# Optimization experiments

Hardware: AMD Instinct MI355X
Metric: run time of the kernel (lower is better)

## Reference

```python
import jax, jax.numpy as jnp
import numpy as np

PAIR = 128
HID = 64
EPS = 1e-5


def _ln(x, w, b):
    mu = jnp.mean(x, axis=-1, keepdims=True)
    var = jnp.mean((x - mu) ** 2, axis=-1, keepdims=True)
    return (x - mu) * jax.lax.rsqrt(var + EPS) * w + b


def setup_inputs() -> dict:
    key = jax.random.key(0)
    ks = jax.random.split(key, 8)
    B, N = 1, 448
    s_in = 1.0 / np.sqrt(PAIR)
    s_h = 1.0 / np.sqrt(HID)
    return {
        "z": jax.random.normal(ks[0], (B, N, N, PAIR), jnp.float32),
        "z_mask": jnp.ones((B, N, N), jnp.float32),
        "ln_w": jnp.ones((PAIR,), jnp.float32),
        "ln_b": jnp.zeros((PAIR,), jnp.float32),
        "lnh_w": jnp.ones((HID,), jnp.float32),
        "lnh_b": jnp.zeros((HID,), jnp.float32),
        "g1_w": jax.random.uniform(ks[1], (PAIR, HID), jnp.float32, -s_in, s_in),
        "g1_b": jnp.zeros((HID,), jnp.float32),
        "g2_w": jax.random.uniform(ks[2], (PAIR, HID), jnp.float32, -s_in, s_in),
        "g2_b": jnp.zeros((HID,), jnp.float32),
        "l1_w": jax.random.uniform(ks[3], (PAIR, HID), jnp.float32, -s_in, s_in),
        "l1_b": jnp.zeros((HID,), jnp.float32),
        "l2_w": jax.random.uniform(ks[4], (PAIR, HID), jnp.float32, -s_in, s_in),
        "l2_b": jnp.zeros((HID,), jnp.float32),
        "eg_w": jax.random.uniform(ks[5], (PAIR, PAIR), jnp.float32, -s_in, s_in),
        "eg_b": jnp.zeros((PAIR,), jnp.float32),
        "out_w": jax.random.uniform(ks[6], (HID, PAIR), jnp.float32, -s_h, s_h),
        "out_b": jnp.zeros((PAIR,), jnp.float32),
    }


def reference(z, z_mask, ln_w, ln_b, lnh_w, lnh_b, g1_w, g1_b, g2_w, g2_b,
              l1_w, l1_b, l2_w, l2_b, eg_w, eg_b, out_w, out_b):
    m = z_mask[..., None]                      # [B,N,N,1]
    zn = _ln(z, ln_w, ln_b)                    # [B,N,N,P]
    ab1 = jax.nn.sigmoid(zn @ g1_w + g1_b) * (zn @ l1_w + l1_b) * m  # [B,N,N,H]
    ab2 = jax.nn.sigmoid(zn @ g2_w + g2_b) * (zn @ l2_w + l2_b) * m  # [B,N,N,H]
    # outgoing + incoming triangle products, per channel c
    block = (jnp.einsum('bikc,bjkc->bijc', ab1, ab2)
             + jnp.einsum('bkic,bkjc->bijc', ab1, ab2))              # [B,N,N,H]
    out = jax.nn.sigmoid(zn @ eg_w + eg_b) * (_ln(block, lnh_w, lnh_b) @ out_w + out_b) * m
    return out
```

## Files before the change

### kernel.cpp

```cpp
#include <hip/hip_runtime.h>
#include <stdint.h>

#define N 448
#define NN (N*N)
#define P 128
#define H 64
#define PN 512
#define CH (PN*N)

typedef __attribute__((ext_vector_type(8))) short bf16x8;
typedef __attribute__((ext_vector_type(4))) float f32x4;
typedef __attribute__((ext_vector_type(16))) float f32x16;

__device__ __forceinline__ ushort f2bf(float f) {
    uint u = __builtin_bit_cast(uint, f);
    uint r = u + 0x7FFFu + ((u >> 16) & 1u);
    return (ushort)(r >> 16);
}
__device__ __forceinline__ float bf2f(ushort h) {
    uint u = ((uint)h) << 16;
    return __builtin_bit_cast(float, u);
}
__device__ __forceinline__ float sigmoidf(float x) {
    return 1.0f / (1.0f + __expf(-x));
}
__device__ __forceinline__ uint cvtpk(float lo, float hi) {
    uint r;
    asm("v_cvt_pk_bf16_f32 %0, %1, %2" : "=v"(r) : "v"(lo), "v"(hi));
    return r;
}

__global__ void k_prep(const float* __restrict__ g1w, const float* __restrict__ l1w,
                       const float* __restrict__ g2w, const float* __restrict__ l2w,
                       const float* __restrict__ egw,
                       ushort* __restrict__ wfrag) {
    int idx = blockIdx.x*256 + threadIdx.x;
    for (int e = idx; e < 24*4*64*8; e += gridDim.x*256) {
        int b  = e & 7;
        int l  = (e >> 3) & 63;
        int ks = (e >> 9) & 3;
        int ct = e >> 11;
        int k   = ks*32 + 8*(l>>4) + b;
        int col = ct*16 + (l & 15);
        float v;
        if (col < 64)       v = g1w[k*64 + col];
        else if (col < 128) v = l1w[k*64 + col - 64];
        else if (col < 192) v = g2w[k*64 + col - 128];
        else if (col < 256) v = l2w[k*64 + col - 192];
        else                v = egw[k*128 + col - 256];
        wfrag[e] = f2bf(v);
    }
}

__global__ __launch_bounds__(256) void k_proj(
    const float* __restrict__ z, const float* __restrict__ mask,
    const float* __restrict__ lnw, const float* __restrict__ lnb,
    const float* __restrict__ g1b, const float* __restrict__ l1b,
    const float* __restrict__ g2b, const float* __restrict__ l2b,
    const float* __restrict__ egb,
    const ushort* __restrict__ wfrag,
    ushort* __restrict__ abt, ushort* __restrict__ gsig)
{
    __shared__ ushort zn[64*128];
    __shared__ ushort abstage[128*72];
    const int t = threadIdx.x;
    const int w = t >> 6, l = t & 63;
    const int i = blockIdx.x / 7, j0 = (blockIdx.x % 7) * 64;

    {
        const int p = t >> 2;
        const int q = t & 3;
        const float* zp = z + (size_t)(i*N + j0 + p)*P + q*32;
        float4 v[8];
        #pragma unroll
        for (int x = 0; x < 8; ++x) v[x] = *(const float4*)(zp + x*4);
        float s = 0.f, sq = 0.f;
        #pragma unroll
        for (int x = 0; x < 8; ++x) {
            s  += v[x].x + v[x].y + v[x].z + v[x].w;
            sq += v[x].x*v[x].x + v[x].y*v[x].y + v[x].z*v[x].z + v[x].w*v[x].w;
        }
        s += __shfl_xor(s, 1);  sq += __shfl_xor(sq, 1);
        s += __shfl_xor(s, 2);  sq += __shfl_xor(sq, 2);
        float mu   = s * (1.0f/128.0f);
        float var  = sq * (1.0f/128.0f) - mu*mu;
        float rstd = rsqrtf(var + 1e-5f);
        #pragma unroll
        for (int cc = 0; cc < 4; ++cc) {
            int chunk = q*4 + cc;
            const float* lwp = lnw + chunk*8;
            const float* lbp = lnb + chunk*8;
            float4 lwa = *(const float4*)(lwp), lwb = *(const float4*)(lwp+4);
            float4 lba = *(const float4*)(lbp), lbb = *(const float4*)(lbp+4);
            float4 va = v[cc*2], vb = v[cc*2+1];
            float n0 = (va.x - mu)*rstd*lwa.x + lba.x;
            float n1 = (va.y - mu)*rstd*lwa.y + lba.y;
            float n2 = (va.z - mu)*rstd*lwa.z + lba.z;
            float n3 = (va.w - mu)*rstd*lwa.w + lba.w;
            float n4 = (vb.x - mu)*rstd*lwb.x + lbb.x;
            float n5 = (vb.y - mu)*rstd*lwb.y + lbb.y;
            float n6 = (vb.z - mu)*rstd*lwb.z + lbb.z;
            float n7 = (vb.w - mu)*rstd*lwb.w + lbb.w;
            uint4 pk;
            pk.x = cvtpk(n0, n1);
            pk.y = cvtpk(n2, n3);
            pk.z = cvtpk(n4, n5);
            pk.w = cvtpk(n6, n7);
            uint boff = (uint)p*256u + (((uint)(chunk ^ (p & 7)) & 15u) << 4);
            *(uint4*)((char*)zn + boff) = pk;
        }
    }
    __syncthreads();

    const int half = w & 1, pair = w >> 1;
    const uint lr = l & 15, lk = l >> 4;
    const float* mrow = mask + (size_t)i*N + j0;
    const float* gb = pair ? g2b : g1b;
    const float* lb = pair ? l2b : l1b;

    float4 mv4[4];
    #pragma unroll
    for (int mi = 0; mi < 4; ++mi) mv4[mi] = *(const float4*)(mrow + mi*16 + (int)lk*4);

    #pragma unroll 1
    for (int sub = 0; sub < 2; ++sub) {
        const int ctg = pair*8 + half*2 + sub;
        const int ctl = ctg + 4;
        f32x4 ag[4], al[4];
        #pragma unroll
        for (int mi = 0; mi < 4; ++mi) { ag[mi] = (f32x4){0,0,0,0}; al[mi] = (f32x4){0,0,0,0}; }

        #pragma unroll
        for (int ks = 0; ks < 4; ++ks) {
            bf16x8 bg  = *(const bf16x8*)(wfrag + ((size_t)(ctg*4 + ks)*64 + l)*8);
            bf16x8 blf = *(const bf16x8*)(wfrag + ((size_t)(ctl*4 + ks)*64 + l)*8);
            #pragma unroll
            for (int mi = 0; mi < 4; ++mi) {
                uint row = mi*16u + lr;
                uint chunk = (uint)(ks*4) + lk;
                bf16x8 af = *(const bf16x8*)((const char*)zn + row*256u + (((chunk ^ (row & 7u)) & 15u) << 4));
                ag[mi] = __builtin_amdgcn_mfma_f32_16x16x32_bf16(af, bg,  ag[mi], 0,0,0);
                al[mi] = __builtin_amdgcn_mfma_f32_16x16x32_bf16(af, blf, al[mi], 0,0,0);
            }
        }

        const int cidx = (half*2 + sub)*16 + (int)lr;
        const float gbias = gb[cidx];
        const float lbias = lb[cidx];
        const int srow = pair*64 + cidx;
        #pragma unroll
        for (int mi = 0; mi < 4; ++mi) {
            float4 mv = mv4[mi];
            float o0 = sigmoidf(ag[mi][0] + gbias) * (al[mi][0] + lbias) * mv.x;
            float o1 = sigmoidf(ag[mi][1] + gbias) * (al[mi][1] + lbias) * mv.y;
            float o2 = sigmoidf(ag[mi][2] + gbias) * (al[mi][2] + lbias) * mv.z;
            float o3 = sigmoidf(ag[mi][3] + gbias) * (al[mi][3] + lbias) * mv.w;
            uint2 pk;
            pk.x = cvtpk(o0, o1);
            pk.y = cvtpk(o2, o3);
            *(uint2*)(abstage + (size_t)srow*72 + mi*16 + (int)lk*4) = pk;
        }
    }
    __syncthreads();

    {
        int r = t >> 1, hh2 = t & 1;
        const ushort* sp = abstage + (size_t)r*72 + hh2*32;
        ushort* dp = abt + (size_t)r*CH + (size_t)i*N + j0 + hh2*32;
        #pragma unroll
        for (int k2 = 0; k2 < 4; ++k2) {
            uint4 vv = *(const uint4*)(sp + k2*8);
            *(uint4*)(dp + k2*8) = vv;
        }
    }

    {
        f32x4 ae[4][2];
        #pragma unroll
        for (int mi = 0; mi < 4; ++mi) { ae[mi][0] = (f32x4){0,0,0,0}; ae[mi][1] = (f32x4){0,0,0,0}; }

        #pragma unroll
        for (int ks = 0; ks < 4; ++ks) {
            bf16x8 b0 = *(const bf16x8*)(wfrag + ((size_t)((16 + w*2)*4 + ks)*64 + l)*8);
            bf16x8 b1 = *(const bf16x8*)(wfrag + ((size_t)((17 + w*2)*4 + ks)*64 + l)*8);
            #pragma unroll
            for (int mi = 0; mi < 4; ++mi) {
                uint row = mi*16u + lr;
                uint chunk = (uint)(ks*4) + lk;
                bf16x8 af = *(const bf16x8*)((const char*)zn + row*256u + (((chunk ^ (row & 7u)) & 15u) << 4));
                ae[mi][0] = __builtin_amdgcn_mfma_f32_16x16x32_bf16(af, b0, ae[mi][0], 0,0,0);
                ae[mi][1] = __builtin_amdgcn_mfma_f32_16x16x32_bf16(af, b1, ae[mi][1], 0,0,0);
            }
        }

        __syncthreads();

        float biasB[2];
        biasB[0] = egb[w*32 + (int)lr];
        biasB[1] = egb[w*32 + 16 + (int)lr];
        #pragma unroll
        for (int mi = 0; mi < 4; ++mi) {
            float4 mv = mv4[mi];
            float mva[4] = { mv.x, mv.y, mv.z, mv.w };
            #pragma unroll
            for (int e = 0; e < 2; ++e) {
                uint cg = (uint)(w*32 + e*16) + lr;
                #pragma unroll
                for (int r = 0; r < 4; ++r) {
                    float sg = sigmoidf(ae[mi][e][r] + biasB[e]) * mva[r];
                    uint row = (uint)(mi*16) + lk*4u + (uint)r;
                    uint boff = row*256u + (((((cg >> 3) ^ (row & 7u)) & 15u)) << 4) + ((cg & 7u) << 1);
                    *(ushort*)((char*)zn + boff) = (ushort)cvtpk(sg, sg);
                }
            }
        }
    }
    __syncthreads();

    {
        int p2 = t >> 2, q2 = t & 3;
        size_t pos = (size_t)(i*N + j0 + p2);
        #pragma unroll
        for (int s2 = 0; s2 < 4; ++s2) {
            int chunk = q2*4 + s2;
            uint boff = (uint)p2*256u + (((uint)(chunk ^ (p2 & 7)) & 15u) << 4);
            uint4 vv = *(const uint4*)((const char*)zn + boff);
            *(uint4*)(gsig + pos*128 + q2*32 + s2*8) = vv;
        }
    }
}

__global__ __launch_bounds__(256) void k_transpose(const ushort* __restrict__ abt,
                                                   ushort* __restrict__ abtt) {
    int bid = blockIdx.x;
    int tile = bid % 49, a = bid / 49;
    int y0 = (tile / 7) * 64, x0 = (tile % 7) * 64;
    const ushort* src = abt  + (size_t)a*CH;
    ushort*       dst = abtt + (size_t)a*CH;
    __shared__ ushort tl[64][68];
    int t = threadIdx.x;
    #pragma unroll
    for (int q = 0; q < 4; ++q) {
        int f = q*1024 + t*4;
        int r = f >> 6, c4 = f & 63;
        ushort4 v = *(const ushort4*)(src + (size_t)(y0 + r)*N + x0 + c4);
        tl[r][c4] = v.x; tl[r][c4+1] = v.y; tl[r][c4+2] = v.z; tl[r][c4+3] = v.w;
    }
    __syncthreads();
    #pragma unroll
    for (int q = 0; q < 4; ++q) {
        int f = q*1024 + t*4;
        int r = f >> 6, c4 = f & 63;
        ushort4 v;
        v.x = tl[c4][r]; v.y = tl[c4+1][r]; v.z = tl[c4+2][r]; v.w = tl[c4+3][r];
        *(ushort4*)(dst + (size_t)(x0 + r)*N + y0 + c4) = v;
    }
}

__global__ __launch_bounds__(256) void k_tri(const ushort* __restrict__ abt,
                                             const ushort* __restrict__ abtt,
                                             float* __restrict__ blk) {
    int bid = (blockIdx.x & 7)*128 + (blockIdx.x >> 3);
    const int c = bid >> 4;
    const int tij = bid & 15;
    const int i0 = (tij >> 2) * 128, j0 = (tij & 3) * 128;
    const int t = threadIdx.x, w = t >> 6, l = t & 63;
    const int wr = w >> 1, wc = w & 1;
    const uint l31 = l & 31, kg = (uint)l >> 5;

    __shared__ ushort lds[4][128*64];

    const ushort* basep = (w >= 2) ? abtt : abt;
    const int chan = (w & 1) ? 64 + c : c;
    const int r0   = (w & 1) ? j0 : i0;
    const ushort* sbase = basep + (size_t)chan*CH + (size_t)r0*N;

    f32x16 acc[2][2];
    #pragma unroll
    for (int a = 0; a < 2; ++a)
        #pragma unroll
        for (int b = 0; b < 2; ++b) acc[a][b] = (f32x16){0,0,0,0,0,0,0,0,0,0,0,0,0,0,0,0};

    for (int kk = 0; kk < 7; ++kk) {
        __syncthreads();
        const ushort* sb = sbase + kk*64;
        #pragma unroll
        for (int q = 0; q < 16; ++q) {
            int r  = q*8 + (l >> 3);
            int ch = (l & 7) ^ (r & 7);
            const ushort* g = sb + (size_t)r*N + ch*8;
            __builtin_amdgcn_global_load_lds(
                (const __attribute__((address_space(1))) uint*)g,
                (__attribute__((address_space(3))) uint*)(&lds[w][q*512]),
                16, 0, 0);
        }
        __syncthreads();

        #pragma unroll
        for (int ks = 0; ks < 4; ++ks) {
            const uint chunk = (uint)(ks*2) + kg;
            {
                bf16x8 aA[2], bB[2];
                #pragma unroll
                for (int x = 0; x < 2; ++x) {
                    uint rowa = (uint)wr*64u + (uint)x*32u + l31;
                    uint rowb = (uint)wc*64u + (uint)x*32u + l31;
                    aA[x] = *(const bf16x8*)((const char*)lds[0] + rowa*128u + (((chunk ^ (rowa & 7u)) & 15u) << 4));
                    bB[x] = *(const bf16x8*)((const char*)lds[1] + rowb*128u + (((chunk ^ (rowb & 7u)) & 15u) << 4));
                }
                #pragma unroll
                for (int ra = 0; ra < 2; ++ra)
                    #pragma unroll
                    for (int cb = 0; cb < 2; ++cb)
                        acc[ra][cb] = __builtin_amdgcn_mfma_f32_32x32x16_bf16(aA[ra], bB[cb], acc[ra][cb], 0,0,0);
            }
            {
                bf16x8 aA[2], bB[2];
                #pragma unroll
                for (int x = 0; x < 2; ++x) {
                    uint rowa = (uint)wr*64u + (uint)x*32u + l31;
                    uint rowb = (uint)wc*64u + (uint)x*32u + l31;
                    aA[x] = *(const bf16x8*)((const char*)lds[2] + rowa*128u + (((chunk ^ (rowa & 7u)) & 15u) << 4));
                    bB[x] = *(const bf16x8*)((const char*)lds[3] + rowb*128u + (((chunk ^ (rowb & 7u)) & 15u) << 4));
                }
                #pragma unroll
                for (int ra = 0; ra < 2; ++ra)
                    #pragma unroll
                    for (int cb = 0; cb < 2; ++cb)
                        acc[ra][cb] = __builtin_amdgcn_mfma_f32_32x32x16_bf16(aA[ra], bB[cb], acc[ra][cb], 0,0,0);
            }
        }
    }

    #pragma unroll
    for (int ra = 0; ra < 2; ++ra) {
        #pragma unroll
        for (int cb = 0; cb < 2; ++cb) {
            int jb = j0 + wc*64 + cb*32 + (int)l31;
            if (jb < N) {
                #pragma unroll
                for (int r = 0; r < 16; ++r) {
                    int ii = i0 + wr*64 + ra*32 + (r & 3) + 8*(r >> 2) + 4*(int)kg;
                    if (ii < N) blk[(size_t)c*NN + (size_t)ii*N + jb] = acc[ra][cb][r];
                }
            }
        }
    }
}

__global__ __launch_bounds__(256) void k_out(const float* __restrict__ blk,
    const ushort* __restrict__ gsig,
    const float* __restrict__ lnhw, const float* __restrict__ lnhb,
    const float* __restrict__ outw, const float* __restrict__ outb,
    float* __restrict__ out)
{
    __shared__ float sblk[2][64][68];
    const int t = threadIdx.x;
    const int w = t >> 6, l = t & 63;
    const int base = blockIdx.x * 256;

    float4 pre[4];
    #pragma unroll
    for (int qq = 0; qq < 4; ++qq) {
        int flat = qq*256 + t;
        int h = flat >> 4, f4 = flat & 15;
        pre[qq] = *(const float4*)(blk + (size_t)h*NN + base + f4*4);
    }

    #pragma unroll 1
    for (int tt = 0; tt < 4; ++tt) {
        const int b = tt & 1;
        const int pos0 = base + tt*64;

        #pragma unroll
        for (int qq = 0; qq < 4; ++qq) {
            int flat = qq*256 + t;
            int h = flat >> 4, f4 = flat & 15;
            sblk[b][f4*4+0][h] = pre[qq].x;
            sblk[b][f4*4+1][h] = pre[qq].y;
            sblk[b][f4*4+2][h] = pre[qq].z;
            sblk[b][f4*4+3][h] = pre[qq].w;
        }
        if (tt < 3) {
            #pragma unroll
            for (int qq = 0; qq < 4; ++qq) {
                int flat = qq*256 + t;
                int h = flat >> 4, f4 = flat & 15;
                pre[qq] = *(const float4*)(blk + (size_t)h*NN + pos0 + 64 + f4*4);
            }
        }
        __syncthreads();

        {
            int p = w*16 + (l >> 2);
            int sub = l & 3;
            float vv[16];
            float s = 0.f, sq = 0.f;
            #pragma unroll
            for (int j = 0; j < 16; ++j) {
                float x = sblk[b][p][sub*16 + j];
                vv[j] = x; s += x; sq += x*x;
            }
            s += __shfl_xor(s, 1);  sq += __shfl_xor(sq, 1);
            s += __shfl_xor(s, 2);  sq += __shfl_xor(sq, 2);
            float mu   = s * (1.0f/64.0f);
            float var  = sq * (1.0f/64.0f) - mu*mu;
            float rstd = rsqrtf(var + 1e-5f);
            #pragma unroll
            for (int j = 0; j < 16; ++j) {
                float nv = (vv[j] - mu)*rstd*lnhw[sub*16+j] + lnhb[sub*16+j];
                sblk[b][p][sub*16 + j] = nv;
            }
        }
        __syncthreads();

        const int c4 = (t & 31) * 4;
        const int pg = t >> 5;
        float4 ob = *(const float4*)(outb + c4);

        #pragma unroll 1
        for (int hh = 0; hh < 2; ++hh) {
            const int prow = hh*32 + pg*4;
            float acc[4][4];
            #pragma unroll
            for (int j2 = 0; j2 < 4; ++j2)
                #pragma unroll
                for (int cc = 0; cc < 4; ++cc) acc[j2][cc] = 0.f;

            #pragma unroll 4
            for (int h4 = 0; h4 < 16; ++h4) {
                float4 wv[4];
                #pragma unroll
                for (int j = 0; j < 4; ++j)
                    wv[j] = *(const float4*)(outw + (h4*4+j)*128 + c4);
                #pragma unroll
                for (int j2 = 0; j2 < 4; ++j2) {
                    float4 av = *(const float4*)(&sblk[b][prow + j2][h4*4]);
                    acc[j2][0] += av.x*wv[0].x + av.y*wv[1].x + av.z*wv[2].x + av.w*wv[3].x;
                    acc[j2][1] += av.x*wv[0].y + av.y*wv[1].y + av.z*wv[2].y + av.w*wv[3].y;
                    acc[j2][2] += av.x*wv[0].z + av.y*wv[1].z + av.z*wv[2].z + av.w*wv[3].z;
                    acc[j2][3] += av.x*wv[0].w + av.y*wv[1].w + av.z*wv[2].w + av.w*wv[3].w;
                }
            }

            #pragma unroll
            for (int j2 = 0; j2 < 4; ++j2) {
                size_t pos = (size_t)(pos0 + prow + j2);
                ushort4 gv = *(const ushort4*)(gsig + pos*128 + c4);
                float4 res;
                res.x = bf2f(gv.x) * (acc[j2][0] + ob.x);
                res.y = bf2f(gv.y) * (acc[j2][1] + ob.y);
                res.z = bf2f(gv.z) * (acc[j2][2] + ob.z);
                res.w = bf2f(gv.w) * (acc[j2][3] + ob.w);
                *(float4*)(out + pos*128 + c4) = res;
            }
        }
    }
}

extern "C" void kernel_launch(void* const* d_in, const int* in_sizes, int n_in,
                              void* d_out, int out_size, void* d_ws, size_t ws_size,
                              hipStream_t stream) {
    const float* z    = (const float*)d_in[0];
    const float* mask = (const float*)d_in[1];
    const float* lnw  = (const float*)d_in[2];
    const float* lnb  = (const float*)d_in[3];
    const float* lnhw = (const float*)d_in[4];
    const float* lnhb = (const float*)d_in[5];
    const float* g1w  = (const float*)d_in[6];
    const float* g1b  = (const float*)d_in[7];
    const float* g2w  = (const float*)d_in[8];
    const float* g2b  = (const float*)d_in[9];
    const float* l1w  = (const float*)d_in[10];
    const float* l1b  = (const float*)d_in[11];
    const float* l2w  = (const float*)d_in[12];
    const float* l2b  = (const float*)d_in[13];
    const float* egw  = (const float*)d_in[14];
    const float* egb  = (const float*)d_in[15];
    const float* outw = (const float*)d_in[16];
    const float* outb = (const float*)d_in[17];

    char* ws = (char*)d_ws;
    const size_t SZ_AB = (size_t)2*64*CH*2;
    const size_t SZ_G  = (size_t)NN*128*2;
    const size_t SZ_BL = (size_t)64*NN*4;
    ushort* abt    = (ushort*)ws;
    ushort* abtt   = (ushort*)(ws + SZ_AB);
    ushort* gsig   = (ushort*)(ws + 2*SZ_AB);
    float*  blkb   = (float*) (ws + 2*SZ_AB + SZ_G);
    ushort* wfrag  = (ushort*)(ws + 2*SZ_AB + SZ_G + SZ_BL);

    k_prep<<<32, 256, 0, stream>>>(g1w, l1w, g2w, l2w, egw, wfrag);
    k_proj<<<3136, 256, 0, stream>>>(z, mask, lnw, lnb, g1b, l1b, g2b, l2b, egb, wfrag, abt, gsig);
    k_transpose<<<128*49, 256, 0, stream>>>(abt, abtt);
    k_tri<<<64*16, 256, 0, stream>>>(abt, abtt, blkb);
    k_out<<<NN/256, 256, 0, stream>>>(blkb, gsig, lnhw, lnhb, outw, outb, (float*)d_out);
}
```

Measured before the change: 290.2 us.

## Make k_proj persistent per row with register prefetch of next z tile

k_proj now launches one block per row i (448 blocks) and loops over the 7 column tiles internally, instead of one block per 64-column tile. The next tile's z values are loaded into registers while the current tile is normalized and projected, and the LayerNorm weights and eg bias are loaded once per block. The aim is to hide global load latency and amortize per-block setup. The cost is fewer blocks (448 on a many-CU GPU, so lower occupancy and parallelism), an extra barrier per iteration, and higher register pressure from the prefetch buffer.

```diff
diff --git a/kernel.cpp b/kernel.cpp
--- a/kernel.cpp
+++ b/kernel.cpp
@@ -65,168 +65,187 @@
     __shared__ ushort abstage[128*72];
     const int t = threadIdx.x;
     const int w = t >> 6, l = t & 63;
-    const int i = blockIdx.x / 7, j0 = (blockIdx.x % 7) * 64;
-
-    {
-        const int p = t >> 2;
-        const int q = t & 3;
-        const float* zp = z + (size_t)(i*N + j0 + p)*P + q*32;
-        float4 v[8];
-        #pragma unroll
-        for (int x = 0; x < 8; ++x) v[x] = *(const float4*)(zp + x*4);
-        float s = 0.f, sq = 0.f;
-        #pragma unroll
-        for (int x = 0; x < 8; ++x) {
-            s  += v[x].x + v[x].y + v[x].z + v[x].w;
-            sq += v[x].x*v[x].x + v[x].y*v[x].y + v[x].z*v[x].z + v[x].w*v[x].w;
-        }
-        s += __shfl_xor(s, 1);  sq += __shfl_xor(sq, 1);
-        s += __shfl_xor(s, 2);  sq += __shfl_xor(sq, 2);
-        float mu   = s * (1.0f/128.0f);
-        float var  = sq * (1.0f/128.0f) - mu*mu;
-        float rstd = rsqrtf(var + 1e-5f);
-        #pragma unroll
-        for (int cc = 0; cc < 4; ++cc) {
-            int chunk = q*4 + cc;
-            const float* lwp = lnw + chunk*8;
-            const float* lbp = lnb + chunk*8;
-            float4 lwa = *(const float4*)(lwp), lwb = *(const float4*)(lwp+4);
-            float4 lba = *(const float4*)(lbp), lbb = *(const float4*)(lbp+4);
-            float4 va = v[cc*2], vb = v[cc*2+1];
-            float n0 = (va.x - mu)*rstd*lwa.x + lba.x;
-            float n1 = (va.y - mu)*rstd*lwa.y + lba.y;
-            float n2 = (va.z - mu)*rstd*lwa.z + lba.z;
-            float n3 = (va.w - mu)*rstd*lwa.w + lba.w;
-            float n4 = (vb.x - mu)*rstd*lwb.x + lbb.x;
-            float n5 = (vb.y - mu)*rstd*lwb.y + lbb.y;
-            float n6 = (vb.z - mu)*rstd*lwb.z + lbb.z;
-            float n7 = (vb.w - mu)*rstd*lwb.w + lbb.w;
-            uint4 pk;
-            pk.x = cvtpk(n0, n1);
-            pk.y = cvtpk(n2, n3);
-            pk.z = cvtpk(n4, n5);
-            pk.w = cvtpk(n6, n7);
-            uint boff = (uint)p*256u + (((uint)(chunk ^ (p & 7)) & 15u) << 4);
-            *(uint4*)((char*)zn + boff) = pk;
-        }
-    }
-    __syncthreads();
-
+    const int i = blockIdx.x;
+
+    const int p = t >> 2;
+    const int q = t & 3;
     const int half = w & 1, pair = w >> 1;
     const uint lr = l & 15, lk = l >> 4;
-    const float* mrow = mask + (size_t)i*N + j0;
     const float* gb = pair ? g2b : g1b;
     const float* lb = pair ? l2b : l1b;
 
-    float4 mv4[4];
+    float4 lwa[4], lwb[4], lba[4], lbb[4];
     #pragma unroll
-    for (int mi = 0; mi < 4; ++mi) mv4[mi] = *(const float4*)(mrow + mi*16 + (int)lk*4);
+    for (int cc = 0; cc < 4; ++cc) {
+        int chunk = q*4 + cc;
+        lwa[cc] = *(const float4*)(lnw + chunk*8);
+        lwb[cc] = *(const float4*)(lnw + chunk*8 + 4);
+        lba[cc] = *(const float4*)(lnb + chunk*8);
+        lbb[cc] = *(const float4*)(lnb + chunk*8 + 4);
+    }
+    float egb0 = egb[w*32 + (int)lr];
+    float egb1 = egb[w*32 + 16 + (int)lr];
+
+    float4 vA[8];
+    {
+        const float* zp = z + (size_t)(i*N + p)*P + q*32;
+        #pragma unroll
+        for (int x = 0; x < 8; ++x) vA[x] = *(const float4*)(zp + x*4);
+    }
 
     #pragma unroll 1
-    for (int sub = 0; sub < 2; ++sub) {
-        const int ctg = pair*8 + half*2 + sub;
-        const int ctl = ctg + 4;
-        f32x4 ag[4], al[4];
-        #pragma unroll
-        for (int mi = 0; mi < 4; ++mi) { ag[mi] = (f32x4){0,0,0,0}; al[mi] = (f32x4){0,0,0,0}; }
-
-        #pragma unroll
-        for (int ks = 0; ks < 4; ++ks) {
-            bf16x8 bg  = *(const bf16x8*)(wfrag + ((size_t)(ctg*4 + ks)*64 + l)*8);
-            bf16x8 blf = *(const bf16x8*)(wfrag + ((size_t)(ctl*4 + ks)*64 + l)*8);
+    for (int jt = 0; jt < 7; ++jt) {
+        const int j0 = jt*64;
+        const float* mrow = mask + (size_t)i*N + j0;
+
+        {
+            float s = 0.f, sq = 0.f;
+            #pragma unroll
+            for (int x = 0; x < 8; ++x) {
+                s  += vA[x].x + vA[x].y + vA[x].z + vA[x].w;
+                sq += vA[x].x*vA[x].x + vA[x].y*vA[x].y + vA[x].z*vA[x].z + vA[x].w*vA[x].w;
+            }
+            s += __shfl_xor(s, 1);  sq += __shfl_xor(sq, 1);
+            s += __shfl_xor(s, 2);  sq += __shfl_xor(sq, 2);
+            float mu   = s * (1.0f/128.0f);
+            float var  = sq * (1.0f/128.0f) - mu*mu;
+            float rstd = rsqrtf(var + 1e-5f);
+            #pragma unroll
+            for (int cc = 0; cc < 4; ++cc) {
+                int chunk = q*4 + cc;
+                float4 va = vA[cc*2], vb = vA[cc*2+1];
+                float n0 = (va.x - mu)*rstd*lwa[cc].x + lba[cc].x;
+                float n1 = (va.y - mu)*rstd*lwa[cc].y + lba[cc].y;
+                float n2 = (va.z - mu)*rstd*lwa[cc].z + lba[cc].z;
+                float n3 = (va.w - mu)*rstd*lwa[cc].w + lba[cc].w;
+                float n4 = (vb.x - mu)*rstd*lwb[cc].x + lbb[cc].x;
+                float n5 = (vb.y - mu)*rstd*lwb[cc].y + lbb[cc].y;
+                float n6 = (vb.z - mu)*rstd*lwb[cc].z + lbb[cc].z;
+                float n7 = (vb.w - mu)*rstd*lwb[cc].w + lbb[cc].w;
+                uint4 pk;
+                pk.x = cvtpk(n0, n1);
+                pk.y = cvtpk(n2, n3);
+                pk.z = cvtpk(n4, n5);
+                pk.w = cvtpk(n6, n7);
+                uint boff = (uint)p*256u + (((uint)(chunk ^ (p & 7)) & 15u) << 4);
+                *(uint4*)((char*)zn + boff) = pk;
+            }
+        }
+        if (jt < 6) {
+            const float* zp = z + (size_t)(i*N + j0 + 64 + p)*P + q*32;
+            #pragma unroll
+            for (int x = 0; x < 8; ++x) vA[x] = *(const float4*)(zp + x*4);
+        }
+        __syncthreads();
+
+        float4 mv4[4];
+        #pragma unroll
+        for (int mi = 0; mi < 4; ++mi) mv4[mi] = *(const float4*)(mrow + mi*16 + (int)lk*4);
+
+        #pragma unroll 1
+        for (int sub = 0; sub < 2; ++sub) {
+            const int ctg = pair*8 + half*2 + sub;
+            const int ctl = ctg + 4;
+            f32x4 ag[4], al[4];
+            #pragma unroll
+            for (int mi = 0; mi < 4; ++mi) { ag[mi] = (f32x4){0,0,0,0}; al[mi] = (f32x4){0,0,0,0}; }
+
+            #pragma unroll
+            for (int ks = 0; ks < 4; ++ks) {
+                bf16x8 bg  = *(const bf16x8*)(wfrag + ((size_t)(ctg*4 + ks)*64 + l)*8);
+                bf16x8 blf = *(const bf16x8*)(wfrag + ((size_t)(ctl*4 + ks)*64 + l)*8);
+                #pragma unroll
+                for (int mi = 0; mi < 4; ++mi) {
+                    uint row = mi*16u + lr;
+                    uint chunk = (uint)(ks*4) + lk;
+                    bf16x8 af = *(const bf16x8*)((const char*)zn + row*256u + (((chunk ^ (row & 7u)) & 15u) << 4));
+                    ag[mi] = __builtin_amdgcn_mfma_f32_16x16x32_bf16(af, bg,  ag[mi], 0,0,0);
+                    al[mi] = __builtin_amdgcn_mfma_f32_16x16x32_bf16(af, blf, al[mi], 0,0,0);
+                }
+            }
+
+            const int cidx = (half*2 + sub)*16 + (int)lr;
+            const float gbias = gb[cidx];
+            const float lbias = lb[cidx];
+            const int srow = pair*64 + cidx;
             #pragma unroll
             for (int mi = 0; mi < 4; ++mi) {
-                uint row = mi*16u + lr;
-                uint chunk = (uint)(ks*4) + lk;
-                bf16x8 af = *(const bf16x8*)((const char*)zn + row*256u + (((chunk ^ (row & 7u)) & 15u) << 4));
-                ag[mi] = __builtin_amdgcn_mfma_f32_16x16x32_bf16(af, bg,  ag[mi], 0,0,0);
-                al[mi] = __builtin_amdgcn_mfma_f32_16x16x32_bf16(af, blf, al[mi], 0,0,0);
-            }
-        }
-
-        const int cidx = (half*2 + sub)*16 + (int)lr;
-        const float gbias = gb[cidx];
-        const float lbias = lb[cidx];
-        const int srow = pair*64 + cidx;
-        #pragma unroll
-        for (int mi = 0; mi < 4; ++mi) {
-            float4 mv = mv4[mi];
-            float o0 = sigmoidf(ag[mi][0] + gbias) * (al[mi][0] + lbias) * mv.x;
-            float o1 = sigmoidf(ag[mi][1] + gbias) * (al[mi][1] + lbias) * mv.y;
-            float o2 = sigmoidf(ag[mi][2] + gbias) * (al[mi][2] + lbias) * mv.z;
-            float o3 = sigmoidf(ag[mi][3] + gbias) * (al[mi][3] + lbias) * mv.w;
-            uint2 pk;
-            pk.x = cvtpk(o0, o1);
-            pk.y = cvtpk(o2, o3);
-            *(uint2*)(abstage + (size_t)srow*72 + mi*16 + (int)lk*4) = pk;
-        }
-    }
-    __syncthreads();
-
-    {
-        int r = t >> 1, hh2 = t & 1;
-        const ushort* sp = abstage + (size_t)r*72 + hh2*32;
-        ushort* dp = abt + (size_t)r*CH + (size_t)i*N + j0 + hh2*32;
-        #pragma unroll
-        for (int k2 = 0; k2 < 4; ++k2) {
-            uint4 vv = *(const uint4*)(sp + k2*8);
-            *(uint4*)(dp + k2*8) = vv;
-        }
-    }
-
-    {
-        f32x4 ae[4][2];
-        #pragma unroll
-        for (int mi = 0; mi < 4; ++mi) { ae[mi][0] = (f32x4){0,0,0,0}; ae[mi][1] = (f32x4){0,0,0,0}; }
-
-        #pragma unroll
-        for (int ks = 0; ks < 4; ++ks) {
-            bf16x8 b0 = *(const bf16x8*)(wfrag + ((size_t)((16 + w*2)*4 + ks)*64 + l)*8);
-            bf16x8 b1 = *(const bf16x8*)(wfrag + ((size_t)((17 + w*2)*4 + ks)*64 + l)*8);
+                float4 mv = mv4[mi];
+                float o0 = sigmoidf(ag[mi][0] + gbias) * (al[mi][0] + lbias) * mv.x;
+                float o1 = sigmoidf(ag[mi][1] + gbias) * (al[mi][1] + lbias) * mv.y;
+                float o2 = sigmoidf(ag[mi][2] + gbias) * (al[mi][2] + lbias) * mv.z;
+                float o3 = sigmoidf(ag[mi][3] + gbias) * (al[mi][3] + lbias) * mv.w;
+                uint2 pk;
+                pk.x = cvtpk(o0, o1);
+                pk.y = cvtpk(o2, o3);
+                *(uint2*)(abstage + (size_t)srow*72 + mi*16 + (int)lk*4) = pk;
+            }
+        }
+        __syncthreads();
+
+        {
+            int r = t >> 1, hh2 = t & 1;
+            const ushort* sp = abstage + (size_t)r*72 + hh2*32;
+            ushort* dp = abt + (size_t)r*CH + (size_t)i*N + j0 + hh2*32;
+            #pragma unroll
+            for (int k2 = 0; k2 < 4; ++k2) {
+                uint4 vv = *(const uint4*)(sp + k2*8);
+                *(uint4*)(dp + k2*8) = vv;
+            }
+        }
+
+        {
+            f32x4 ae[4][2];
+            #pragma unroll
+            for (int mi = 0; mi < 4; ++mi) { ae[mi][0] = (f32x4){0,0,0,0}; ae[mi][1] = (f32x4){0,0,0,0}; }
+
+            #pragma unroll
+            for (int ks = 0; ks < 4; ++ks) {
+                bf16x8 b0 = *(const bf16x8*)(wfrag + ((size_t)((16 + w*2)*4 + ks)*64 + l)*8);
+                bf16x8 b1 = *(const bf16x8*)(wfrag + ((size_t)((17 + w*2)*4 + ks)*64 + l)*8);
+                #pragma unroll
+                for (int mi = 0; mi < 4; ++mi) {
+                    uint row = mi*16u + lr;
+                    uint chunk = (uint)(ks*4) + lk;
+                    bf16x8 af = *(const bf16x8*)((const char*)zn + row*256u + (((chunk ^ (row & 7u)) & 15u) << 4));
+                    ae[mi][0] = __builtin_amdgcn_mfma_f32_16x16x32_bf16(af, b0, ae[mi][0], 0,0,0);
+                    ae[mi][1] = __builtin_amdgcn_mfma_f32_16x16x32_bf16(af, b1, ae[mi][1], 0,0,0);
+                }
+            }
+
+            __syncthreads();
+
             #pragma unroll
             for (int mi = 0; mi < 4; ++mi) {
-                uint row = mi*16u + lr;
-                uint chunk = (uint)(ks*4) + lk;
-                bf16x8 af = *(const bf16x8*)((const char*)zn + row*256u + (((chunk ^ (row & 7u)) & 15u) << 4));
-                ae[mi][0] = __builtin_amdgcn_mfma_f32_16x16x32_bf16(af, b0, ae[mi][0], 0,0,0);
-                ae[mi][1] = __builtin_amdgcn_mfma_f32_16x16x32_bf16(af, b1, ae[mi][1], 0,0,0);
-            }
-        }
-
-        __syncthreads();
-
-        float biasB[2];
-        biasB[0] = egb[w*32 + (int)lr];
-        biasB[1] = egb[w*32 + 16 + (int)lr];
-        #pragma unroll
-        for (int mi = 0; mi < 4; ++mi) {
-            float4 mv = mv4[mi];
-            float mva[4] = { mv.x, mv.y, mv.z, mv.w };
-            #pragma unroll
-            for (int e = 0; e < 2; ++e) {
-                uint cg = (uint)(w*32 + e*16) + lr;
-                #pragma unroll
-                for (int r = 0; r < 4; ++r) {
-                    float sg = sigmoidf(ae[mi][e][r] + biasB[e]) * mva[r];
-                    uint row = (uint)(mi*16) + lk*4u + (uint)r;
-                    uint boff = row*256u + (((((cg >> 3) ^ (row & 7u)) & 15u)) << 4) + ((cg & 7u) << 1);
-                    *(ushort*)((char*)zn + boff) = (ushort)cvtpk(sg, sg);
-                }
-            }
-        }
-    }
-    __syncthreads();
-
-    {
-        int p2 = t >> 2, q2 = t & 3;
-        size_t pos = (size_t)(i*N + j0 + p2);
-        #pragma unroll
-        for (int s2 = 0; s2 < 4; ++s2) {
-            int chunk = q2*4 + s2;
-            uint boff = (uint)p2*256u + (((uint)(chunk ^ (p2 & 7)) & 15u) << 4);
-            uint4 vv = *(const uint4*)((const char*)zn + boff);
-            *(uint4*)(gsig + pos*128 + q2*32 + s2*8) = vv;
-        }
+                float4 mv = mv4[mi];
+                float mva[4] = { mv.x, mv.y, mv.z, mv.w };
+                #pragma unroll
+                for (int e = 0; e < 2; ++e) {
+                    uint cg = (uint)(w*32 + e*16) + lr;
+                    float bias = e ? egb1 : egb0;
+                    #pragma unroll
+                    for (int r = 0; r < 4; ++r) {
+                        float sg = sigmoidf(ae[mi][e][r] + bias) * mva[r];
+                        uint row = (uint)(mi*16) + lk*4u + (uint)r;
+                        uint boff = row*256u + (((((cg >> 3) ^ (row & 7u)) & 15u)) << 4) + ((cg & 7u) << 1);
+                        *(ushort*)((char*)zn + boff) = (ushort)cvtpk(sg, sg);
+                    }
+                }
+            }
+        }
+        __syncthreads();
+
+        {
+            size_t pos = (size_t)(i*N + j0 + p);
+            #pragma unroll
+            for (int s2 = 0; s2 < 4; ++s2) {
+                int chunk = q*4 + s2;
+                uint boff = (uint)p*256u + (((uint)(chunk ^ (p & 7)) & 15u) << 4);
+                uint4 vv = *(const uint4*)((const char*)zn + boff);
+                *(uint4*)(gsig + pos*128 + q*32 + s2*8) = vv;
+            }
+        }
+        __syncthreads();
     }
 }
 
@@ -491,7 +510,7 @@
     ushort* wfrag  = (ushort*)(ws + 2*SZ_AB + SZ_G + SZ_BL);
 
     k_prep<<<32, 256, 0, stream>>>(g1w, l1w, g2w, l2w, egw, wfrag);
-    k_proj<<<3136, 256, 0, stream>>>(z, mask, lnw, lnb, g1b, l1b, g2b, l2b, egb, wfrag, abt, gsig);
+    k_proj<<<448, 256, 0, stream>>>(z, mask, lnw, lnb, g1b, l1b, g2b, l2b, egb, wfrag, abt, gsig);
     k_transpose<<<128*49, 256, 0, stream>>>(abt, abtt);
     k_tri<<<64*16, 256, 0, stream>>>(abt, abtt, blkb);
     k_out<<<NN/256, 256, 0, stream>>>(blkb, gsig, lnhw, lnhb, outw, outb, (float*)d_out);
```

New measurement: 315.1 us. 1.09x slower.

## Restructure projection kernel into single-wave blocks with register-held A fragments

Applied to the files above, without the earlier changes.

The projection kernel now runs one 64-thread wave per block over 32 rows instead of four waves over 64 rows. Each wave keeps its LayerNorm'd A fragments in registers and computes every gate, linear and eg column tile itself. The shared-memory staging buffer for the ab output is dropped, so ab values go straight to global memory as 8-byte stores. This aims to cut LDS use and inter-wave barriers and to raise occupancy. In exchange, each wave reloads the full weight-fragment set, which raises cache traffic, and the global ab stores are narrower and less coalesced.

```diff
diff --git a/kernel.cpp b/kernel.cpp
--- a/kernel.cpp
+++ b/kernel.cpp
@@ -52,7 +52,7 @@
     }
 }
 
-__global__ __launch_bounds__(256) void k_proj(
+__global__ __launch_bounds__(64) void k_proj(
     const float* __restrict__ z, const float* __restrict__ mask,
     const float* __restrict__ lnw, const float* __restrict__ lnb,
     const float* __restrict__ g1b, const float* __restrict__ l1b,
@@ -61,16 +61,18 @@
     const ushort* __restrict__ wfrag,
     ushort* __restrict__ abt, ushort* __restrict__ gsig)
 {
-    __shared__ ushort zn[64*128];
-    __shared__ ushort abstage[128*72];
-    const int t = threadIdx.x;
-    const int w = t >> 6, l = t & 63;
-    const int i = blockIdx.x / 7, j0 = (blockIdx.x % 7) * 64;
-
-    {
-        const int p = t >> 2;
-        const int q = t & 3;
-        const float* zp = z + (size_t)(i*N + j0 + p)*P + q*32;
+    __shared__ ushort zn[32*128];
+    const int l = threadIdx.x;
+    const int bid = blockIdx.x;
+    const int i = bid / 14, j0 = (bid % 14) * 32;
+    const uint lr = l & 15, lk = (uint)l >> 4;
+    const int pp = l >> 2;
+    const int pq = l & 3;
+
+    #pragma unroll 1
+    for (int px = 0; px < 2; ++px) {
+        int p = px*16 + pp;
+        const float* zp = z + (size_t)(i*N + j0 + p)*P + pq*32;
         float4 v[8];
         #pragma unroll
         for (int x = 0; x < 8; ++x) v[x] = *(const float4*)(zp + x*4);
@@ -87,7 +89,7 @@
         float rstd = rsqrtf(var + 1e-5f);
         #pragma unroll
         for (int cc = 0; cc < 4; ++cc) {
-            int chunk = q*4 + cc;
+            int chunk = pq*4 + cc;
             const float* lwp = lnw + chunk*8;
             const float* lbp = lnb + chunk*8;
             float4 lwa = *(const float4*)(lwp), lwb = *(const float4*)(lwp+4);
@@ -112,102 +114,92 @@
     }
     __syncthreads();
 
-    const int half = w & 1, pair = w >> 1;
-    const uint lr = l & 15, lk = l >> 4;
-    const float* mrow = mask + (size_t)i*N + j0;
-    const float* gb = pair ? g2b : g1b;
-    const float* lb = pair ? l2b : l1b;
-
-    float4 mv4[4];
-    #pragma unroll
-    for (int mi = 0; mi < 4; ++mi) mv4[mi] = *(const float4*)(mrow + mi*16 + (int)lk*4);
+    bf16x8 af[2][4];
+    #pragma unroll
+    for (int mi = 0; mi < 2; ++mi) {
+        uint row = (uint)mi*16u + lr;
+        #pragma unroll
+        for (int ks = 0; ks < 4; ++ks) {
+            uint chunk = (uint)(ks*4) + lk;
+            af[mi][ks] = *(const bf16x8*)((const char*)zn + row*256u + (((chunk ^ (row & 7u)) & 15u) << 4));
+        }
+    }
+
+    float4 mv4[2];
+    #pragma unroll
+    for (int mi = 0; mi < 2; ++mi)
+        mv4[mi] = *(const float4*)(mask + (size_t)i*N + j0 + mi*16 + (int)lk*4);
 
     #pragma unroll 1
-    for (int sub = 0; sub < 2; ++sub) {
-        const int ctg = pair*8 + half*2 + sub;
-        const int ctl = ctg + 4;
-        f32x4 ag[4], al[4];
-        #pragma unroll
-        for (int mi = 0; mi < 4; ++mi) { ag[mi] = (f32x4){0,0,0,0}; al[mi] = (f32x4){0,0,0,0}; }
-
+    for (int pair = 0; pair < 2; ++pair) {
+        const float* gbp = pair ? g2b : g1b;
+        const float* lbp = pair ? l2b : l1b;
+        #pragma unroll 1
+        for (int sub = 0; sub < 4; ++sub) {
+            const int ctg = pair*8 + sub;
+            const int ctl = ctg + 4;
+            f32x4 ag[2], al[2];
+            ag[0] = (f32x4){0,0,0,0}; ag[1] = (f32x4){0,0,0,0};
+            al[0] = (f32x4){0,0,0,0}; al[1] = (f32x4){0,0,0,0};
+            #pragma unroll
+            for (int ks = 0; ks < 4; ++ks) {
+                bf16x8 bg  = *(const bf16x8*)(wfrag + ((size_t)(ctg*4 + ks)*64 + l)*8);
+                bf16x8 blf = *(const bf16x8*)(wfrag + ((size_t)(ctl*4 + ks)*64 + l)*8);
+                #pragma unroll
+                for (int mi = 0; mi < 2; ++mi) {
+                    ag[mi] = __builtin_amdgcn_mfma_f32_16x16x32_bf16(af[mi][ks], bg,  ag[mi], 0,0,0);
+                    al[mi] = __builtin_amdgcn_mfma_f32_16x16x32_bf16(af[mi][ks], blf, al[mi], 0,0,0);
+                }
+            }
+            const int cidx = sub*16 + (int)lr;
+            const float gbias = gbp[cidx];
+            const float lbias = lbp[cidx];
+            #pragma unroll
+            for (int mi = 0; mi < 2; ++mi) {
+                float4 mv = mv4[mi];
+                float o0 = sigmoidf(ag[mi][0] + gbias) * (al[mi][0] + lbias) * mv.x;
+                float o1 = sigmoidf(ag[mi][1] + gbias) * (al[mi][1] + lbias) * mv.y;
+                float o2 = sigmoidf(ag[mi][2] + gbias) * (al[mi][2] + lbias) * mv.z;
+                float o3 = sigmoidf(ag[mi][3] + gbias) * (al[mi][3] + lbias) * mv.w;
+                uint2 pk;
+                pk.x = cvtpk(o0, o1);
+                pk.y = cvtpk(o2, o3);
+                size_t off = (size_t)(pair*64 + cidx)*CH + (size_t)i*N + j0 + mi*16 + (int)lk*4;
+                *(uint2*)(abt + off) = pk;
+            }
+        }
+    }
+
+    #pragma unroll 1
+    for (int es = 0; es < 4; ++es) {
+        const int ct0 = 16 + es*2;
+        f32x4 ae0[2], ae1[2];
+        ae0[0] = (f32x4){0,0,0,0}; ae0[1] = (f32x4){0,0,0,0};
+        ae1[0] = (f32x4){0,0,0,0}; ae1[1] = (f32x4){0,0,0,0};
         #pragma unroll
         for (int ks = 0; ks < 4; ++ks) {
-            bf16x8 bg  = *(const bf16x8*)(wfrag + ((size_t)(ctg*4 + ks)*64 + l)*8);
-            bf16x8 blf = *(const bf16x8*)(wfrag + ((size_t)(ctl*4 + ks)*64 + l)*8);
-            #pragma unroll
-            for (int mi = 0; mi < 4; ++mi) {
-                uint row = mi*16u + lr;
-                uint chunk = (uint)(ks*4) + lk;
-                bf16x8 af = *(const bf16x8*)((const char*)zn + row*256u + (((chunk ^ (row & 7u)) & 15u) << 4));
-                ag[mi] = __builtin_amdgcn_mfma_f32_16x16x32_bf16(af, bg,  ag[mi], 0,0,0);
-                al[mi] = __builtin_amdgcn_mfma_f32_16x16x32_bf16(af, blf, al[mi], 0,0,0);
-            }
-        }
-
-        const int cidx = (half*2 + sub)*16 + (int)lr;
-        const float gbias = gb[cidx];
-        const float lbias = lb[cidx];
-        const int srow = pair*64 + cidx;
-        #pragma unroll
-        for (int mi = 0; mi < 4; ++mi) {
-            float4 mv = mv4[mi];
-            float o0 = sigmoidf(ag[mi][0] + gbias) * (al[mi][0] + lbias) * mv.x;
-            float o1 = sigmoidf(ag[mi][1] + gbias) * (al[mi][1] + lbias) * mv.y;
-            float o2 = sigmoidf(ag[mi][2] + gbias) * (al[mi][2] + lbias) * mv.z;
-            float o3 = sigmoidf(ag[mi][3] + gbias) * (al[mi][3] + lbias) * mv.w;
-            uint2 pk;
-            pk.x = cvtpk(o0, o1);
-            pk.y = cvtpk(o2, o3);
-            *(uint2*)(abstage + (size_t)srow*72 + mi*16 + (int)lk*4) = pk;
-        }
-    }
-    __syncthreads();
-
-    {
-        int r = t >> 1, hh2 = t & 1;
-        const ushort* sp = abstage + (size_t)r*72 + hh2*32;
-        ushort* dp = abt + (size_t)r*CH + (size_t)i*N + j0 + hh2*32;
-        #pragma unroll
-        for (int k2 = 0; k2 < 4; ++k2) {
-            uint4 vv = *(const uint4*)(sp + k2*8);
-            *(uint4*)(dp + k2*8) = vv;
-        }
-    }
-
-    {
-        f32x4 ae[4][2];
-        #pragma unroll
-        for (int mi = 0; mi < 4; ++mi) { ae[mi][0] = (f32x4){0,0,0,0}; ae[mi][1] = (f32x4){0,0,0,0}; }
-
-        #pragma unroll
-        for (int ks = 0; ks < 4; ++ks) {
-            bf16x8 b0 = *(const bf16x8*)(wfrag + ((size_t)((16 + w*2)*4 + ks)*64 + l)*8);
-            bf16x8 b1 = *(const bf16x8*)(wfrag + ((size_t)((17 + w*2)*4 + ks)*64 + l)*8);
-            #pragma unroll
-            for (int mi = 0; mi < 4; ++mi) {
-                uint row = mi*16u + lr;
-                uint chunk = (uint)(ks*4) + lk;
-                bf16x8 af = *(const bf16x8*)((const char*)zn + row*256u + (((chunk ^ (row & 7u)) & 15u) << 4));
-                ae[mi][0] = __builtin_amdgcn_mfma_f32_16x16x32_bf16(af, b0, ae[mi][0], 0,0,0);
-                ae[mi][1] = __builtin_amdgcn_mfma_f32_16x16x32_bf16(af, b1, ae[mi][1], 0,0,0);
-            }
-        }
-
-        __syncthreads();
-
-        float biasB[2];
-        biasB[0] = egb[w*32 + (int)lr];
-        biasB[1] = egb[w*32 + 16 + (int)lr];
-        #pragma unroll
-        for (int mi = 0; mi < 4; ++mi) {
+            bf16x8 b0 = *(const bf16x8*)(wfrag + ((size_t)(ct0*4 + ks)*64 + l)*8);
+            bf16x8 b1 = *(const bf16x8*)(wfrag + ((size_t)((ct0+1)*4 + ks)*64 + l)*8);
+            #pragma unroll
+            for (int mi = 0; mi < 2; ++mi) {
+                ae0[mi] = __builtin_amdgcn_mfma_f32_16x16x32_bf16(af[mi][ks], b0, ae0[mi], 0,0,0);
+                ae1[mi] = __builtin_amdgcn_mfma_f32_16x16x32_bf16(af[mi][ks], b1, ae1[mi], 0,0,0);
+            }
+        }
+        float bias0 = egb[es*32 + (int)lr];
+        float bias1 = egb[es*32 + 16 + (int)lr];
+        #pragma unroll
+        for (int mi = 0; mi < 2; ++mi) {
             float4 mv = mv4[mi];
             float mva[4] = { mv.x, mv.y, mv.z, mv.w };
             #pragma unroll
             for (int e = 0; e < 2; ++e) {
-                uint cg = (uint)(w*32 + e*16) + lr;
+                uint cg = (uint)(es*32 + e*16) + lr;
+                float bias = e ? bias1 : bias0;
+                const f32x4* aep = e ? &ae1[mi] : &ae0[mi];
                 #pragma unroll
                 for (int r = 0; r < 4; ++r) {
-                    float sg = sigmoidf(ae[mi][e][r] + biasB[e]) * mva[r];
+                    float sg = sigmoidf((*aep)[r] + bias) * mva[r];
                     uint row = (uint)(mi*16) + lk*4u + (uint)r;
                     uint boff = row*256u + (((((cg >> 3) ^ (row & 7u)) & 15u)) << 4) + ((cg & 7u) << 1);
                     *(ushort*)((char*)zn + boff) = (ushort)cvtpk(sg, sg);
@@ -217,15 +209,16 @@
     }
     __syncthreads();
 
-    {
-        int p2 = t >> 2, q2 = t & 3;
-        size_t pos = (size_t)(i*N + j0 + p2);
+    #pragma unroll
+    for (int px = 0; px < 2; ++px) {
+        int p = px*16 + pp;
+        size_t pos = (size_t)(i*N + j0 + p);
         #pragma unroll
         for (int s2 = 0; s2 < 4; ++s2) {
-            int chunk = q2*4 + s2;
-            uint boff = (uint)p2*256u + (((uint)(chunk ^ (p2 & 7)) & 15u) << 4);
+            int chunk = pq*4 + s2;
+            uint boff = (uint)p*256u + (((uint)(chunk ^ (p & 7)) & 15u) << 4);
             uint4 vv = *(const uint4*)((const char*)zn + boff);
-            *(uint4*)(gsig + pos*128 + q2*32 + s2*8) = vv;
+            *(uint4*)(gsig + pos*128 + pq*32 + s2*8) = vv;
         }
     }
 }
@@ -491,7 +484,7 @@
     ushort* wfrag  = (ushort*)(ws + 2*SZ_AB + SZ_G + SZ_BL);
 
     k_prep<<<32, 256, 0, stream>>>(g1w, l1w, g2w, l2w, egw, wfrag);
-    k_proj<<<3136, 256, 0, stream>>>(z, mask, lnw, lnb, g1b, l1b, g2b, l2b, egb, wfrag, abt, gsig);
+    k_proj<<<6272, 64, 0, stream>>>(z, mask, lnw, lnb, g1b, l1b, g2b, l2b, egb, wfrag, abt, gsig);
     k_transpose<<<128*49, 256, 0, stream>>>(abt, abtt);
     k_tri<<<64*16, 256, 0, stream>>>(abt, abtt, blkb);
     k_out<<<NN/256, 256, 0, stream>>>(blkb, gsig, lnhw, lnhb, outw, outb, (float*)d_out);
```

Result: slower. 300.0 us (+3.4%).
